# Optimization experiments

Hardware: AMD Instinct MI355X
Metric: run time of the kernel (lower is better)

Reference implementation:

```python
import jax, jax.numpy as jnp
import numpy as np

IN_F, OUT_F, LAT, RES, K, B = 512, 512, 512, 64, 3, 8
EPS = 1e-08
C_LIN = 1.0 / np.sqrt(LAT)          # EqualizedWeight scale for linear
C_CONV = 1.0 / np.sqrt(IN_F * K * K)  # EqualizedWeight scale for conv


def setup_inputs() -> dict:
    key = jax.random.key(0)
    k1, k2, k3, k4 = jax.random.split(key, 4)
    return {
        "x": jax.random.normal(k1, (B, IN_F, RES, RES), dtype=jnp.float32),
        "latent": jax.random.normal(k2, (B, LAT), dtype=jnp.float32),
        "w_lin": jax.random.normal(k3, (IN_F, LAT), dtype=jnp.float32),
        "b_lin": jnp.ones((IN_F,), dtype=jnp.float32),
        "w_conv": jax.random.normal(k4, (OUT_F, IN_F, K, K), dtype=jnp.float32),
        "b_conv": jnp.zeros((OUT_F,), dtype=jnp.float32),
    }


def reference(x, latent, w_lin, b_lin, w_conv, b_conv):
    # EqualizedLinear: s = latent @ (w_lin*c).T + b_lin*lr_mul  -> [B, IN_F]
    s = latent @ (w_lin * C_LIN).T + b_lin
    # ModulatedConv2d. Per-sample weight w[b,o,i,k,k] = (w_conv*c)[o,i,k,k]*s[b,i],
    # demodulated by sigma_inv[b,o] = rsqrt(sum_{i,k,k} w^2 + eps).
    w = w_conv * C_CONV  # [O, I, K, K]
    # sum_{k,k} w^2 over spatial -> [O, I], then contract with s^2 -> [B, O]
    w2 = jnp.sum(w * w, axis=(2, 3))  # [O, I]
    sigma_inv = jax.lax.rsqrt(jnp.einsum('oi,bi->bo', w2, s * s) + EPS)
    # conv(x, w*s_b) == conv(x * s_b, w): modulate input, single batched conv,
    # then demodulate output per (b, o). Avoids materializing B*O filters.
    x_mod = x * s[:, :, None, None]
    y = jax.lax.conv_general_dilated(
        x_mod, w,
        window_strides=(1, 1),
        padding=[((K - 1) // 2, (K - 1) // 2)] * 2,
        dimension_numbers=('NCHW', 'OIHW', 'NCHW'),
    )
    y = y * sigma_inv[:, :, None, None] + b_conv[None, :, None, None]
    return y
```

## Files before the change

### kernel.cpp

```cpp
#include <hip/hip_runtime.h>
#include <hip/hip_bf16.h>

#define IN_F 512
#define OUT_F 512
#define LATD 512
#define RES 64
#define BATCH 8
#define EPSV 1e-8f

static constexpr float C_LIN  = 0.04419417382415922f;
static constexpr float C_CONV = 0.014731391274719739f;

typedef __attribute__((ext_vector_type(8)))  short short8;
typedef __attribute__((ext_vector_type(16))) float f32x16;

union BF { __hip_bfloat16 h; short s; };

__device__ __forceinline__ void async_load16(const char* g, char* l) {
  __builtin_amdgcn_global_load_lds(
      (const __attribute__((address_space(1))) unsigned int*)g,
      (__attribute__((address_space(3))) unsigned int*)l, 16, 0, 0);
}

__global__ void k_compute_s(const float* __restrict__ latent,
                            const float* __restrict__ w_lin,
                            const float* __restrict__ b_lin,
                            float* __restrict__ s) {
  const int i = blockIdx.x;
  const int lane = threadIdx.x;
  const float4* wl = (const float4*)(w_lin + (size_t)i * LATD);
  const float4 w0 = wl[lane * 2], w1 = wl[lane * 2 + 1];
  float acc[BATCH];
#pragma unroll
  for (int b = 0; b < BATCH; ++b) {
    const float4* lt = (const float4*)(latent + (size_t)b * LATD);
    const float4 l0 = lt[lane * 2], l1 = lt[lane * 2 + 1];
    acc[b] = w0.x * l0.x + w0.y * l0.y + w0.z * l0.z + w0.w * l0.w +
             w1.x * l1.x + w1.y * l1.y + w1.z * l1.z + w1.w * l1.w;
  }
#pragma unroll
  for (int b = 0; b < BATCH; ++b) {
    float v = acc[b];
#pragma unroll
    for (int off = 32; off > 0; off >>= 1) v += __shfl_down(v, off);
    if (lane == 0) s[b * IN_F + i] = v * C_LIN + b_lin[i];
  }
}

__global__ void k_prep_w(const float* __restrict__ w_conv,
                         short* __restrict__ wb,
                         float* __restrict__ w2) {
  const int t = blockIdx.x * 256 + threadIdx.x;
  const int o = t >> 9;
  const int i = t & 511;
  const float* src = w_conv + (size_t)t * 9;
  const int c = i >> 4, half = (i >> 3) & 1, ch = i & 7;
  const int ob = o >> 7, ol = o & 127;
  short* dst = wb + (size_t)(c * 4 + ob) * 18432 + half * 1024 + ol * 8 + ch;
  float sum = 0.f;
#pragma unroll
  for (int tap = 0; tap < 9; ++tap) {
    const float v = src[tap] * C_CONV;
    sum += v * v;
    BF cv; cv.h = __float2bfloat16(v);
    dst[tap * 2048] = cv.s;
  }
  w2[t] = sum;
}

__global__ void k_sigma(const float* __restrict__ w2,
                        const float* __restrict__ s,
                        float* __restrict__ sigma_inv) {
  const int o = blockIdx.x * 4 + (threadIdx.x >> 6);
  const int lane = threadIdx.x & 63;
  float acc[BATCH];
#pragma unroll
  for (int b = 0; b < BATCH; ++b) acc[b] = 0.f;
#pragma unroll
  for (int k = 0; k < 8; ++k) {
    const int i = k * 64 + lane;
    const float w = w2[o * IN_F + i];
#pragma unroll
    for (int b = 0; b < BATCH; ++b) {
      const float sv = s[b * IN_F + i];
      acc[b] += w * sv * sv;
    }
  }
#pragma unroll
  for (int b = 0; b < BATCH; ++b) {
    float v = acc[b];
#pragma unroll
    for (int off = 32; off > 0; off >>= 1) v += __shfl_down(v, off);
    if (lane == 0) sigma_inv[b * OUT_F + o] = rsqrtf(v + EPSV);
  }
}

__global__ void k_zero_border(char* __restrict__ xmp) {
  char* base = xmp + (size_t)blockIdx.x * 139392;
  for (int q = threadIdx.x; q < 520; q += 256) {
    int h, hf, w;
    if (q < 132)      { h = 0;  hf = (q >= 66) ? 1 : 0; w = q - hf * 66; }
    else if (q < 264) { const int r = q - 132; h = 65; hf = (r >= 66) ? 1 : 0; w = r - hf * 66; }
    else              { const int r = q - 264; h = (r >> 2) + 1; hf = (r >> 1) & 1; w = (r & 1) * 65; }
    *(uint4*)(base + ((size_t)(h * 132 + hf * 66 + w)) * 16) = make_uint4(0u, 0u, 0u, 0u);
  }
}

__global__ void k_modulate(const float* __restrict__ x,
                           const float* __restrict__ s,
                           char* __restrict__ xmp) {
  const int h    = blockIdx.x & 63;
  const int ic32 = (blockIdx.x >> 6) & 15;
  const int b    = blockIdx.x >> 10;
  __shared__ float tile[32][65];
  const int tid = threadIdx.x;
  {
    const int il = tid >> 3, w8 = (tid & 7) * 8;
    const int i = ic32 * 32 + il;
    const float sv = s[b * IN_F + i];
    const float* xp = x + (((size_t)(b * IN_F + i) * RES + h) * RES + w8);
    const float4 v0 = *(const float4*)xp;
    const float4 v1 = *(const float4*)(xp + 4);
    tile[il][w8 + 0] = v0.x * sv; tile[il][w8 + 1] = v0.y * sv;
    tile[il][w8 + 2] = v0.z * sv; tile[il][w8 + 3] = v0.w * sv;
    tile[il][w8 + 4] = v1.x * sv; tile[il][w8 + 5] = v1.y * sv;
    tile[il][w8 + 6] = v1.z * sv; tile[il][w8 + 7] = v1.w * sv;
  }
  __syncthreads();
  {
    const int w = tid >> 2, part = tid & 3;
    const int chalf = part >> 1, hf = part & 1;
    short8 pk;
#pragma unroll
    for (int j = 0; j < 8; ++j) {
      BF cv; cv.h = __float2bfloat16(tile[chalf * 16 + hf * 8 + j][w]);
      pk[j] = cv.s;
    }
    const int c = ic32 * 2 + chalf;
    char* dst = xmp + (size_t)(c * 8 + b) * 139392 +
                ((size_t)(h + 1) * 132 + hf * 66 + (w + 1)) * 16;
    *(short8*)dst = pk;
  }
}

__global__ __launch_bounds__(256, 1)
void k_conv(const char* __restrict__ xmp,
            const short* __restrict__ wbg,
            const float* __restrict__ sigma_inv,
            const float* __restrict__ b_conv,
            float* __restrict__ out) {
  __shared__ __align__(16) char lds[115968];
  const int l = blockIdx.x;
  const int ob = (l >> 3) & 3;
  const int b  = l & 7;
  const int h0 = (l >> 5) * 8;
  const int o0 = ob * 128;
  const int tid = threadIdx.x;
  const int wave = tid >> 6, lane = tid & 63;
  const int l31 = lane & 31, half = lane >> 5;

  f32x16 acc[4][4];
#pragma unroll
  for (int i = 0; i < 4; ++i)
#pragma unroll
    for (int j = 0; j < 4; ++j)
#pragma unroll
      for (int r = 0; r < 16; ++r) acc[i][j][r] = 0.f;

  const char* xsrc0 = xmp + (size_t)b * 139392 + (size_t)h0 * 2112;
  const char* wsrc0 = (const char*)wbg + (size_t)ob * 36864;

#pragma unroll
  for (int k = 0; k < 5; ++k) {
    const int j = tid + k * 256;
    async_load16(xsrc0 + j * 16, lds + j * 16);
  }
  if (tid < 40) { const int j = 1280 + tid; async_load16(xsrc0 + j * 16, lds + j * 16); }
#pragma unroll
  for (int k = 0; k < 9; ++k) {
    const int j = tid + k * 256;
    async_load16(wsrc0 + j * 16, lds + 42240 + j * 16);
  }
  __syncthreads();

  for (int ic = 0; ic < 32; ++ic) {
    const int p = ic & 1;
    if (ic + 1 < 32) {
      const char* xs  = xsrc0 + (size_t)(ic + 1) * (8 * 139392);
      const char* wsr = wsrc0 + (size_t)(ic + 1) * (4 * 36864);
      char* xd = lds + (p ^ 1) * 21120;
      char* wd = lds + 42240 + (p ^ 1) * 36864;
#pragma unroll
      for (int k = 0; k < 5; ++k) {
        const int j = tid + k * 256;
        async_load16(xs + j * 16, xd + j * 16);
      }
      if (tid < 40) { const int j = 1280 + tid; async_load16(xs + j * 16, xd + j * 16); }
#pragma unroll
      for (int k = 0; k < 9; ++k) {
        const int j = tid + k * 256;
        async_load16(wsr + j * 16, wd + j * 16);
      }
    }
    const char* xp = lds + p * 21120;
    const char* wp = lds + 42240 + p * 36864;
#pragma unroll
    for (int tap = 0; tap < 9; ++tap) {
      const int dh = tap / 3, dw = tap - dh * 3;
      short8 av[4];
#pragma unroll
      for (int f = 0; f < 4; ++f)
        av[f] = *(const short8*)(wp + tap * 4096 + half * 2048 + (f * 32 + l31) * 16);
#pragma unroll
      for (int tp = 0; tp < 4; ++tp) {
        const int hr = wave * 2 + (tp >> 1) + dh;
        const int wc = (tp & 1) * 32 + dw + l31;
        const short8 bv = *(const short8*)(xp + (hr * 132 + half * 66 + wc) * 16);
#pragma unroll
        for (int f = 0; f < 4; ++f)
          acc[f][tp] = __builtin_amdgcn_mfma_f32_32x32x16_bf16(av[f], bv, acc[f][tp], 0, 0, 0);
      }
    }
    __syncthreads();
  }

#pragma unroll
  for (int f = 0; f < 4; ++f) {
#pragma unroll
    for (int g = 0; g < 4; ++g) {
#pragma unroll
      for (int r = 0; r < 4; ++r) {
        const int o = o0 + f * 32 + r + 8 * g + 4 * half;
        const float sig  = sigma_inv[b * OUT_F + o];
        const float bias = b_conv[o];
        const int reg = g * 4 + r;
#pragma unroll
        for (int tp = 0; tp < 4; ++tp) {
          const int h = h0 + wave * 2 + (tp >> 1);
          const int w = (tp & 1) * 32 + l31;
          out[(((size_t)(b * OUT_F + o) * RES + h) * RES) + w] =
              acc[f][tp][reg] * sig + bias;
        }
      }
    }
  }
}

extern "C" void kernel_launch(void* const* d_in, const int* in_sizes, int n_in,
                              void* d_out, int out_size, void* d_ws, size_t ws_size,
                              hipStream_t stream) {
  const float* x      = (const float*)d_in[0];
  const float* latent = (const float*)d_in[1];
  const float* w_lin  = (const float*)d_in[2];
  const float* b_lin  = (const float*)d_in[3];
  const float* w_conv = (const float*)d_in[4];
  const float* b_conv = (const float*)d_in[5];
  float* out = (float*)d_out;

  char* ws = (char*)d_ws;
  char*  xmp       = ws;
  short* wb        = (short*)(ws + 35684352);
  float* w2        = (float*)(ws + 40402944);
  float* s         = (float*)(ws + 41451520);
  float* sigma_inv = (float*)(ws + 41467904);

  k_compute_s<<<IN_F, 64, 0, stream>>>(latent, w_lin, b_lin, s);
  k_prep_w<<<1024, 256, 0, stream>>>(w_conv, wb, w2);
  k_sigma<<<128, 256, 0, stream>>>(w2, s, sigma_inv);
  k_zero_border<<<256, 256, 0, stream>>>(xmp);
  k_modulate<<<BATCH * 16 * RES, 256, 0, stream>>>(x, s, xmp);
  k_conv<<<256, 256, 0, stream>>>(xmp, wb, sigma_inv, b_conv, out);
}
```

Baseline: 256.1 us.

## Stream conv weights from global into registers and remap blocks per XCD

```diff
diff --git a/kernel.cpp b/kernel.cpp
--- a/kernel.cpp
+++ b/kernel.cpp
@@ -49,14 +49,15 @@
 
 __global__ void k_prep_w(const float* __restrict__ w_conv,
                          short* __restrict__ wb,
-                         float* __restrict__ w2) {
+                         float* __restrict__ w2,
+                         char* __restrict__ xmp) {
   const int t = blockIdx.x * 256 + threadIdx.x;
   const int o = t >> 9;
   const int i = t & 511;
   const float* src = w_conv + (size_t)t * 9;
-  const int c = i >> 4, half = (i >> 3) & 1, ch = i & 7;
+  const int c = i >> 4, hf0 = (i >> 3) & 1, ch = i & 7;
   const int ob = o >> 7, ol = o & 127;
-  short* dst = wb + (size_t)(c * 4 + ob) * 18432 + half * 1024 + ol * 8 + ch;
+  short* dst = wb + (size_t)(c * 4 + ob) * 18432 + hf0 * 1024 + ol * 8 + ch;
   float sum = 0.f;
 #pragma unroll
   for (int tap = 0; tap < 9; ++tap) {
@@ -66,6 +67,17 @@
     dst[tap * 2048] = cv.s;
   }
   w2[t] = sum;
+
+  if (blockIdx.x < 256) {
+    char* base = xmp + (size_t)blockIdx.x * 139392;
+    for (int q = threadIdx.x; q < 520; q += 256) {
+      int h, hf, w;
+      if (q < 132)      { h = 0;  hf = (q >= 66) ? 1 : 0; w = q - hf * 66; }
+      else if (q < 264) { const int r = q - 132; h = 65; hf = (r >= 66) ? 1 : 0; w = r - hf * 66; }
+      else              { const int r = q - 264; h = (r >> 2) + 1; hf = (r >> 1) & 1; w = (r & 1) * 65; }
+      *(uint4*)(base + ((size_t)(h * 132 + hf * 66 + w)) * 16) = make_uint4(0u, 0u, 0u, 0u);
+    }
+  }
 }
 
 __global__ void k_sigma(const float* __restrict__ w2,
@@ -92,17 +104,6 @@
 #pragma unroll
     for (int off = 32; off > 0; off >>= 1) v += __shfl_down(v, off);
     if (lane == 0) sigma_inv[b * OUT_F + o] = rsqrtf(v + EPSV);
-  }
-}
-
-__global__ void k_zero_border(char* __restrict__ xmp) {
-  char* base = xmp + (size_t)blockIdx.x * 139392;
-  for (int q = threadIdx.x; q < 520; q += 256) {
-    int h, hf, w;
-    if (q < 132)      { h = 0;  hf = (q >= 66) ? 1 : 0; w = q - hf * 66; }
-    else if (q < 264) { const int r = q - 132; h = 65; hf = (r >= 66) ? 1 : 0; w = r - hf * 66; }
-    else              { const int r = q - 264; h = (r >> 2) + 1; hf = (r >> 1) & 1; w = (r & 1) * 65; }
-    *(uint4*)(base + ((size_t)(h * 132 + hf * 66 + w)) * 16) = make_uint4(0u, 0u, 0u, 0u);
   }
 }
 
@@ -149,11 +150,13 @@
             const float* __restrict__ sigma_inv,
             const float* __restrict__ b_conv,
             float* __restrict__ out) {
-  __shared__ __align__(16) char lds[115968];
+  __shared__ __align__(16) char lds[42240];
   const int l = blockIdx.x;
-  const int ob = (l >> 3) & 3;
-  const int b  = l & 7;
-  const int h0 = (l >> 5) * 8;
+  const int xcd = l & 7;
+  const int idx = l >> 3;
+  const int ob = xcd >> 1;
+  const int b  = (xcd & 1) * 4 + (idx & 3);
+  const int h0 = (idx >> 2) * 8;
   const int o0 = ob * 128;
   const int tid = threadIdx.x;
   const int wave = tid >> 6, lane = tid & 63;
@@ -168,7 +171,9 @@
       for (int r = 0; r < 16; ++r) acc[i][j][r] = 0.f;
 
   const char* xsrc0 = xmp + (size_t)b * 139392 + (size_t)h0 * 2112;
-  const char* wsrc0 = (const char*)wbg + (size_t)ob * 36864;
+  const char* wlane = (const char*)wbg + (size_t)ob * 36864 + half * 2048 + l31 * 16;
+
+  short8 abuf[3][4];
 
 #pragma unroll
   for (int k = 0; k < 5; ++k) {
@@ -177,48 +182,58 @@
   }
   if (tid < 40) { const int j = 1280 + tid; async_load16(xsrc0 + j * 16, lds + j * 16); }
 #pragma unroll
-  for (int k = 0; k < 9; ++k) {
-    const int j = tid + k * 256;
-    async_load16(wsrc0 + j * 16, lds + 42240 + j * 16);
-  }
+  for (int f = 0; f < 4; ++f)
+    abuf[0][f] = *(const short8*)(wlane + 0 * 4096 + f * 512);
+#pragma unroll
+  for (int f = 0; f < 4; ++f)
+    abuf[1][f] = *(const short8*)(wlane + 3 * 4096 + f * 512);
   __syncthreads();
 
   for (int ic = 0; ic < 32; ++ic) {
     const int p = ic & 1;
     if (ic + 1 < 32) {
-      const char* xs  = xsrc0 + (size_t)(ic + 1) * (8 * 139392);
-      const char* wsr = wsrc0 + (size_t)(ic + 1) * (4 * 36864);
+      const char* xs = xsrc0 + (size_t)(ic + 1) * (8 * 139392);
       char* xd = lds + (p ^ 1) * 21120;
-      char* wd = lds + 42240 + (p ^ 1) * 36864;
 #pragma unroll
       for (int k = 0; k < 5; ++k) {
         const int j = tid + k * 256;
         async_load16(xs + j * 16, xd + j * 16);
       }
       if (tid < 40) { const int j = 1280 + tid; async_load16(xs + j * 16, xd + j * 16); }
-#pragma unroll
-      for (int k = 0; k < 9; ++k) {
-        const int j = tid + k * 256;
-        async_load16(wsr + j * 16, wd + j * 16);
-      }
     }
     const char* xp = lds + p * 21120;
-    const char* wp = lds + 42240 + p * 36864;
-#pragma unroll
-    for (int tap = 0; tap < 9; ++tap) {
-      const int dh = tap / 3, dw = tap - dh * 3;
-      short8 av[4];
-#pragma unroll
-      for (int f = 0; f < 4; ++f)
-        av[f] = *(const short8*)(wp + tap * 4096 + half * 2048 + (f * 32 + l31) * 16);
-#pragma unroll
-      for (int tp = 0; tp < 4; ++tp) {
-        const int hr = wave * 2 + (tp >> 1) + dh;
-        const int wc = (tp & 1) * 32 + dw + l31;
-        const short8 bv = *(const short8*)(xp + (hr * 132 + half * 66 + wc) * 16);
-#pragma unroll
-        for (int f = 0; f < 4; ++f)
-          acc[f][tp] = __builtin_amdgcn_mfma_f32_32x32x16_bf16(av[f], bv, acc[f][tp], 0, 0, 0);
+#pragma unroll
+    for (int dw = 0; dw < 3; ++dw) {
+      short8 brow[4][2];
+#pragma unroll
+      for (int r = 0; r < 4; ++r)
+#pragma unroll
+        for (int tpc = 0; tpc < 2; ++tpc)
+          brow[r][tpc] = *(const short8*)(
+              xp + (((wave * 2 + r) * 132) + half * 66 + tpc * 32 + dw + l31) * 16);
+#pragma unroll
+      for (int dh = 0; dh < 3; ++dh) {
+        const int j = dw * 3 + dh;
+        const int cur = j % 3;
+        {
+          const int jn = j + 2;
+          const int tgt = jn % 3;
+          const int gn = (jn <= 8) ? jn : jn - 9;
+          const int cn = (jn <= 8) ? ic : (ic + 1 < 32 ? ic + 1 : 31);
+          const int tapn = (gn % 3) * 3 + gn / 3;
+#pragma unroll
+          for (int f = 0; f < 4; ++f)
+            abuf[tgt][f] = *(const short8*)(
+                wlane + (size_t)cn * 147456 + tapn * 4096 + f * 512);
+        }
+#pragma unroll
+        for (int tpr = 0; tpr < 2; ++tpr)
+#pragma unroll
+          for (int tpc = 0; tpc < 2; ++tpc)
+#pragma unroll
+            for (int f = 0; f < 4; ++f)
+              acc[f][tpr * 2 + tpc] = __builtin_amdgcn_mfma_f32_32x32x16_bf16(
+                  abuf[cur][f], brow[dh + tpr][tpc], acc[f][tpr * 2 + tpc], 0, 0, 0);
       }
     }
     __syncthreads();
@@ -265,9 +280,8 @@
   float* sigma_inv = (float*)(ws + 41467904);
 
   k_compute_s<<<IN_F, 64, 0, stream>>>(latent, w_lin, b_lin, s);
-  k_prep_w<<<1024, 256, 0, stream>>>(w_conv, wb, w2);
+  k_prep_w<<<1024, 256, 0, stream>>>(w_conv, wb, w2, xmp);
   k_sigma<<<128, 256, 0, stream>>>(w2, s, sigma_inv);
-  k_zero_border<<<256, 256, 0, stream>>>(xmp);
   k_modulate<<<BATCH * 16 * RES, 256, 0, stream>>>(x, s, xmp);
   k_conv<<<256, 256, 0, stream>>>(xmp, wb, sigma_inv, b_conv, out);
 }
```

After: 289.2 us. 1.13x slower.

## Use 8 waves in conv with row-reuse of input across vertical taps; fuse border zeroing

Applied to the files above, without the earlier changes.

```diff
diff --git a/kernel.cpp b/kernel.cpp
--- a/kernel.cpp
+++ b/kernel.cpp
@@ -49,14 +49,15 @@
 
 __global__ void k_prep_w(const float* __restrict__ w_conv,
                          short* __restrict__ wb,
-                         float* __restrict__ w2) {
+                         float* __restrict__ w2,
+                         char* __restrict__ xmp) {
   const int t = blockIdx.x * 256 + threadIdx.x;
   const int o = t >> 9;
   const int i = t & 511;
   const float* src = w_conv + (size_t)t * 9;
-  const int c = i >> 4, half = (i >> 3) & 1, ch = i & 7;
+  const int c = i >> 4, hf0 = (i >> 3) & 1, ch = i & 7;
   const int ob = o >> 7, ol = o & 127;
-  short* dst = wb + (size_t)(c * 4 + ob) * 18432 + half * 1024 + ol * 8 + ch;
+  short* dst = wb + (size_t)(c * 4 + ob) * 18432 + hf0 * 1024 + ol * 8 + ch;
   float sum = 0.f;
 #pragma unroll
   for (int tap = 0; tap < 9; ++tap) {
@@ -66,6 +67,17 @@
     dst[tap * 2048] = cv.s;
   }
   w2[t] = sum;
+
+  if (blockIdx.x < 256) {
+    char* base = xmp + (size_t)blockIdx.x * 139392;
+    for (int q = threadIdx.x; q < 520; q += 256) {
+      int h, hf, w;
+      if (q < 132)      { h = 0;  hf = (q >= 66) ? 1 : 0; w = q - hf * 66; }
+      else if (q < 264) { const int r = q - 132; h = 65; hf = (r >= 66) ? 1 : 0; w = r - hf * 66; }
+      else              { const int r = q - 264; h = (r >> 2) + 1; hf = (r >> 1) & 1; w = (r & 1) * 65; }
+      *(uint4*)(base + ((size_t)(h * 132 + hf * 66 + w)) * 16) = make_uint4(0u, 0u, 0u, 0u);
+    }
+  }
 }
 
 __global__ void k_sigma(const float* __restrict__ w2,
@@ -92,17 +104,6 @@
 #pragma unroll
     for (int off = 32; off > 0; off >>= 1) v += __shfl_down(v, off);
     if (lane == 0) sigma_inv[b * OUT_F + o] = rsqrtf(v + EPSV);
-  }
-}
-
-__global__ void k_zero_border(char* __restrict__ xmp) {
-  char* base = xmp + (size_t)blockIdx.x * 139392;
-  for (int q = threadIdx.x; q < 520; q += 256) {
-    int h, hf, w;
-    if (q < 132)      { h = 0;  hf = (q >= 66) ? 1 : 0; w = q - hf * 66; }
-    else if (q < 264) { const int r = q - 132; h = 65; hf = (r >= 66) ? 1 : 0; w = r - hf * 66; }
-    else              { const int r = q - 264; h = (r >> 2) + 1; hf = (r >> 1) & 1; w = (r & 1) * 65; }
-    *(uint4*)(base + ((size_t)(h * 132 + hf * 66 + w)) * 16) = make_uint4(0u, 0u, 0u, 0u);
   }
 }
 
@@ -143,7 +144,7 @@
   }
 }
 
-__global__ __launch_bounds__(256, 1)
+__global__ __launch_bounds__(512, 2)
 void k_conv(const char* __restrict__ xmp,
             const short* __restrict__ wbg,
             const float* __restrict__ sigma_inv,
@@ -158,10 +159,14 @@
   const int tid = threadIdx.x;
   const int wave = tid >> 6, lane = tid & 63;
   const int l31 = lane & 31, half = lane >> 5;
-
-  f32x16 acc[4][4];
-#pragma unroll
-  for (int i = 0; i < 4; ++i)
+  const int oh = wave >> 2;
+  const int q  = wave & 3;
+  const int r0 = (q >> 1) * 4;
+  const int c0 = (q & 1) * 32;
+
+  f32x16 acc[2][4];
+#pragma unroll
+  for (int i = 0; i < 2; ++i)
 #pragma unroll
     for (int j = 0; j < 4; ++j)
 #pragma unroll
@@ -171,75 +176,83 @@
   const char* wsrc0 = (const char*)wbg + (size_t)ob * 36864;
 
 #pragma unroll
-  for (int k = 0; k < 5; ++k) {
-    const int j = tid + k * 256;
+  for (int k = 0; k < 2; ++k) {
+    const int j = tid + k * 512;
     async_load16(xsrc0 + j * 16, lds + j * 16);
   }
-  if (tid < 40) { const int j = 1280 + tid; async_load16(xsrc0 + j * 16, lds + j * 16); }
-#pragma unroll
-  for (int k = 0; k < 9; ++k) {
-    const int j = tid + k * 256;
+  if (tid < 296) { const int j = 1024 + tid; async_load16(xsrc0 + j * 16, lds + j * 16); }
+#pragma unroll
+  for (int k = 0; k < 4; ++k) {
+    const int j = tid + k * 512;
     async_load16(wsrc0 + j * 16, lds + 42240 + j * 16);
   }
+  if (tid < 256) { const int j = 2048 + tid; async_load16(wsrc0 + j * 16, lds + 42240 + j * 16); }
   __syncthreads();
 
   for (int ic = 0; ic < 32; ++ic) {
     const int p = ic & 1;
     if (ic + 1 < 32) {
       const char* xs  = xsrc0 + (size_t)(ic + 1) * (8 * 139392);
-      const char* wsr = wsrc0 + (size_t)(ic + 1) * (4 * 36864);
+      const char* wsr = wsrc0 + (size_t)(ic + 1) * 147456;
       char* xd = lds + (p ^ 1) * 21120;
       char* wd = lds + 42240 + (p ^ 1) * 36864;
 #pragma unroll
-      for (int k = 0; k < 5; ++k) {
-        const int j = tid + k * 256;
+      for (int k = 0; k < 2; ++k) {
+        const int j = tid + k * 512;
         async_load16(xs + j * 16, xd + j * 16);
       }
-      if (tid < 40) { const int j = 1280 + tid; async_load16(xs + j * 16, xd + j * 16); }
-#pragma unroll
-      for (int k = 0; k < 9; ++k) {
-        const int j = tid + k * 256;
+      if (tid < 296) { const int j = 1024 + tid; async_load16(xs + j * 16, xd + j * 16); }
+#pragma unroll
+      for (int k = 0; k < 4; ++k) {
+        const int j = tid + k * 512;
         async_load16(wsr + j * 16, wd + j * 16);
       }
+      if (tid < 256) { const int j = 2048 + tid; async_load16(wsr + j * 16, wd + j * 16); }
     }
     const char* xp = lds + p * 21120;
     const char* wp = lds + 42240 + p * 36864;
 #pragma unroll
-    for (int tap = 0; tap < 9; ++tap) {
-      const int dh = tap / 3, dw = tap - dh * 3;
-      short8 av[4];
-#pragma unroll
-      for (int f = 0; f < 4; ++f)
-        av[f] = *(const short8*)(wp + tap * 4096 + half * 2048 + (f * 32 + l31) * 16);
-#pragma unroll
-      for (int tp = 0; tp < 4; ++tp) {
-        const int hr = wave * 2 + (tp >> 1) + dh;
-        const int wc = (tp & 1) * 32 + dw + l31;
-        const short8 bv = *(const short8*)(xp + (hr * 132 + half * 66 + wc) * 16);
-#pragma unroll
-        for (int f = 0; f < 4; ++f)
-          acc[f][tp] = __builtin_amdgcn_mfma_f32_32x32x16_bf16(av[f], bv, acc[f][tp], 0, 0, 0);
+    for (int dw = 0; dw < 3; ++dw) {
+      short8 brow[6];
+#pragma unroll
+      for (int rr = 0; rr < 6; ++rr)
+        brow[rr] = *(const short8*)(
+            xp + (((r0 + rr) * 132) + half * 66 + c0 + dw + l31) * 16);
+#pragma unroll
+      for (int dh = 0; dh < 3; ++dh) {
+        const int tap = dh * 3 + dw;
+        short8 a[2];
+#pragma unroll
+        for (int f = 0; f < 2; ++f)
+          a[f] = *(const short8*)(
+              wp + tap * 4096 + half * 2048 + (oh * 64 + f * 32 + l31) * 16);
+#pragma unroll
+        for (int tpr = 0; tpr < 4; ++tpr)
+#pragma unroll
+          for (int f = 0; f < 2; ++f)
+            acc[f][tpr] = __builtin_amdgcn_mfma_f32_32x32x16_bf16(
+                a[f], brow[tpr + dh], acc[f][tpr], 0, 0, 0);
       }
     }
     __syncthreads();
   }
 
 #pragma unroll
-  for (int f = 0; f < 4; ++f) {
+  for (int f = 0; f < 2; ++f) {
 #pragma unroll
     for (int g = 0; g < 4; ++g) {
 #pragma unroll
       for (int r = 0; r < 4; ++r) {
-        const int o = o0 + f * 32 + r + 8 * g + 4 * half;
+        const int o = o0 + oh * 64 + f * 32 + r + 8 * g + 4 * half;
         const float sig  = sigma_inv[b * OUT_F + o];
         const float bias = b_conv[o];
         const int reg = g * 4 + r;
 #pragma unroll
-        for (int tp = 0; tp < 4; ++tp) {
-          const int h = h0 + wave * 2 + (tp >> 1);
-          const int w = (tp & 1) * 32 + l31;
+        for (int tpr = 0; tpr < 4; ++tpr) {
+          const int h = h0 + r0 + tpr;
+          const int w = c0 + l31;
           out[(((size_t)(b * OUT_F + o) * RES + h) * RES) + w] =
-              acc[f][tp][reg] * sig + bias;
+              acc[f][tpr][reg] * sig + bias;
         }
       }
     }
@@ -265,9 +278,8 @@
   float* sigma_inv = (float*)(ws + 41467904);
 
   k_compute_s<<<IN_F, 64, 0, stream>>>(latent, w_lin, b_lin, s);
-  k_prep_w<<<1024, 256, 0, stream>>>(w_conv, wb, w2);
+  k_prep_w<<<1024, 256, 0, stream>>>(w_conv, wb, w2, xmp);
   k_sigma<<<128, 256, 0, stream>>>(w2, s, sigma_inv);
-  k_zero_border<<<256, 256, 0, stream>>>(xmp);
   k_modulate<<<BATCH * 16 * RES, 256, 0, stream>>>(x, s, xmp);
-  k_conv<<<256, 256, 0, stream>>>(xmp, wb, sigma_inv, b_conv, out);
-}
+  k_conv<<<256, 512, 0, stream>>>(xmp, wb, sigma_inv, b_conv, out);
+}
```

Measured after the change: 258.2 us. About the same (+0.8%).
